# Performance work log

Measured on AMD Instinct MI355X. Metric: run time of the kernel, lower is better.

## Reference

```python
import jax, jax.numpy as jnp
import numpy as np
import math

B, S, E, A, H, L, V = 2, 2048, 512, 512, 8, 4, 50257
HD = A // H  # 64 per-head dim (attention_size // n_heads)
PAD = 0
EPS = 1e-5

def _sin_pe():
    pos = np.arange(S)[:, None].astype(np.float32)
    div = np.exp(np.arange(0, E, 2).astype(np.float32) * (-math.log(10000.0) / E))
    pe = np.zeros((S, E), dtype=np.float32)
    pe[:, 0::2] = np.sin(pos * div)
    pe[:, 1::2] = np.cos(pos * div)
    return jnp.asarray(pe)

PE = _sin_pe()

def setup_inputs():
    key = jax.random.key(0)
    ks = jax.random.split(key, 20)
    s = 0.02
    emb = jax.random.normal(ks[0], (V, E), jnp.float32) * s
    emb = emb.at[PAD].set(0.0)  # nn.Embedding padding_idx row is zero
    return {
        "input_ids": jax.random.randint(ks[1], (B, S), 0, V, dtype=jnp.int32),
        "attention_mask": jnp.ones((B, S), jnp.int32),
        "emb": emb,
        "Wq": jax.random.normal(ks[2], (L, H, E, HD), jnp.float32) * s,
        "Wk": jax.random.normal(ks[3], (L, H, E, HD), jnp.float32) * s,
        "Wv": jax.random.normal(ks[4], (L, H, E, HD), jnp.float32) * s,
        "Wo": jax.random.normal(ks[5], (L, A, E), jnp.float32) * s,
        "ln1_g": jnp.ones((L, E), jnp.float32),
        "ln1_b": jnp.zeros((L, E), jnp.float32),
        "ln2_g": jnp.ones((L, E), jnp.float32),
        "ln2_b": jnp.zeros((L, E), jnp.float32),
        "ff_w1": jax.random.normal(ks[6], (L, E, 4 * E), jnp.float32) * s,
        "ff_b1": jnp.zeros((L, 4 * E), jnp.float32),
        "ff_w2": jax.random.normal(ks[7], (L, 4 * E, E), jnp.float32) * s,
        "ff_b2": jnp.zeros((L, E), jnp.float32),
        "lnf_g": jnp.ones((E,), jnp.float32),
        "lnf_b": jnp.zeros((E,), jnp.float32),
        "Wout": jax.random.normal(ks[8], (E, V), jnp.float32) * s,
        "bout": jnp.zeros((V,), jnp.float32),
    }

def _ln(x, g, b):
    m = jnp.mean(x, axis=-1, keepdims=True)
    v = jnp.mean((x - m) ** 2, axis=-1, keepdims=True)
    return (x - m) / jnp.sqrt(v + EPS) * g + b

def reference(input_ids, attention_mask, emb, Wq, Wk, Wv, Wo, ln1_g, ln1_b, ln2_g, ln2_b, ff_w1, ff_b1, ff_w2, ff_b2, lnf_g, lnf_b, Wout, bout):
    # mask: padding (attention_mask==0) broadcast over queries, OR causal upper triangle
    pad = (attention_mask == 0)[:, None, :]                  # [B,1,S]
    causal = jnp.triu(jnp.ones((S, S), bool), 1)             # [S,S]
    mask = (pad | causal)[:, None, :, :]                     # [B,1,S,S]
    x = emb[input_ids] + PE[None, :S]                        # [B,S,E]
    scale = 1.0 / math.sqrt(HD)

    def block(x, p):
        wq, wk, wv, wo, g1, b1, g2, b2, w1, c1, w2, c2 = p
        xn = _ln(x, g1, b1)
        q = jnp.einsum('bse,hed->bhsd', xn, wq)
        k = jnp.einsum('bse,hed->bhsd', xn, wk)
        v = jnp.einsum('bse,hed->bhsd', xn, wv)
        scores = jnp.einsum('bhsd,bhtd->bhst', q, k) * scale  # masked_fill(-inf) then /sqrt(dk) == mask after scale
        scores = jnp.where(mask, -jnp.inf, scores)
        p_attn = jax.nn.softmax(scores, axis=-1)
        attn = jnp.einsum('bhst,bhtd->bhsd', p_attn, v)
        attn = attn.transpose(0, 2, 1, 3).reshape(B, S, A)    # concat heads
        x = x + attn @ wo                                     # residual + out proj (no bias)
        xn2 = _ln(x, g2, b2)
        h = jax.nn.gelu(xn2 @ w1 + c1, approximate=False)     # nn.GELU default (erf)
        x = x + h @ w2 + c2
        return x, None

    params = (Wq, Wk, Wv, Wo, ln1_g, ln1_b, ln2_g, ln2_b, ff_w1, ff_b1, ff_w2, ff_b2)
    x, _ = jax.lax.scan(block, x, params)
    return _ln(x, lnf_g, lnf_b) @ Wout + bout                 # [B,S,V]
```

## Files before the change

### kernel.cpp

```cpp
#include <hip/hip_runtime.h>
#include <math.h>

#define BB 2
#define SS 2048
#define EE 512
#define HH 8
#define HD 64
#define LL 4
#define VV 50257
#define NTOK (BB*SS)
#define VPAD2 50432

typedef __bf16 bf16_t;
typedef bf16_t bf16x8 __attribute__((ext_vector_type(8)));
typedef float  f32x4  __attribute__((ext_vector_type(4)));

__device__ __forceinline__ void gload_lds16(const void* g, void* l) {
  __builtin_amdgcn_global_load_lds(
      (const __attribute__((address_space(1))) void*)g,
      (__attribute__((address_space(3))) void*)l, 16, 0, 0);
}

__global__ __launch_bounds__(256) void embed_ln_kernel(
    const int* __restrict__ ids, const float* __restrict__ emb,
    const float* __restrict__ g, const float* __restrict__ b,
    float* __restrict__ x, bf16_t* __restrict__ xn) {
  int wv = threadIdx.x >> 6, lane = threadIdx.x & 63;
  int row = blockIdx.x * 4 + wv;
  int s = row & (SS - 1);
  int id = ids[row];
  const float* er = emb + (size_t)id * EE;
  float v[8];
  float sum = 0.f;
#pragma unroll
  for (int j = 0; j < 8; j++) {
    int e = lane * 8 + j;
    float freq = __expf((float)(e & ~1) * -0.01798894604f);
    float ang  = (float)s * freq;
    float pe   = (e & 1) ? __cosf(ang) : __sinf(ang);
    v[j] = er[e] + pe;
    sum += v[j];
  }
  float4* xp = reinterpret_cast<float4*>(x + (size_t)row * EE + lane * 8);
  xp[0] = make_float4(v[0], v[1], v[2], v[3]);
  xp[1] = make_float4(v[4], v[5], v[6], v[7]);
#pragma unroll
  for (int o = 32; o > 0; o >>= 1) sum += __shfl_xor(sum, o);
  float mean = sum * (1.f / EE);
  float var = 0.f;
#pragma unroll
  for (int j = 0; j < 8; j++) { float d = v[j] - mean; var += d * d; }
#pragma unroll
  for (int o = 32; o > 0; o >>= 1) var += __shfl_xor(var, o);
  float inv = rsqrtf(var * (1.f / EE) + 1e-5f);
  bf16_t tmp[8];
#pragma unroll
  for (int j = 0; j < 8; j++) {
    int e = lane * 8 + j;
    tmp[j] = (bf16_t)((v[j] - mean) * inv * g[e] + b[e]);
  }
  *reinterpret_cast<bf16x8*>(xn + (size_t)row * EE + lane * 8) = *reinterpret_cast<bf16x8*>(tmp);
}

__global__ __launch_bounds__(256) void ln_kernel(const float* __restrict__ in,
                                                 bf16_t* __restrict__ out,
                                                 const float* __restrict__ g,
                                                 const float* __restrict__ b) {
  int wv = threadIdx.x >> 6, lane = threadIdx.x & 63;
  int row = blockIdx.x * 4 + wv;
  const float4* r = reinterpret_cast<const float4*>(in + (size_t)row * EE) + lane * 2;
  float4 v0 = r[0], v1 = r[1];
  float s = v0.x + v0.y + v0.z + v0.w + v1.x + v1.y + v1.z + v1.w;
#pragma unroll
  for (int o = 32; o > 0; o >>= 1) s += __shfl_xor(s, o);
  float mean = s * (1.f / EE);
  float d0 = v0.x-mean, d1 = v0.y-mean, d2 = v0.z-mean, d3 = v0.w-mean;
  float d4 = v1.x-mean, d5 = v1.y-mean, d6 = v1.z-mean, d7 = v1.w-mean;
  float var = d0*d0+d1*d1+d2*d2+d3*d3+d4*d4+d5*d5+d6*d6+d7*d7;
#pragma unroll
  for (int o = 32; o > 0; o >>= 1) var += __shfl_xor(var, o);
  float inv = rsqrtf(var * (1.f / EE) + 1e-5f);
  const float4* gp = reinterpret_cast<const float4*>(g) + lane * 2;
  const float4* bp = reinterpret_cast<const float4*>(b) + lane * 2;
  float4 g0 = gp[0], g1 = gp[1], b0 = bp[0], b1 = bp[1];
  bf16_t tmp[8];
  tmp[0] = (bf16_t)(d0*inv*g0.x + b0.x); tmp[1] = (bf16_t)(d1*inv*g0.y + b0.y);
  tmp[2] = (bf16_t)(d2*inv*g0.z + b0.z); tmp[3] = (bf16_t)(d3*inv*g0.w + b0.w);
  tmp[4] = (bf16_t)(d4*inv*g1.x + b1.x); tmp[5] = (bf16_t)(d5*inv*g1.y + b1.y);
  tmp[6] = (bf16_t)(d6*inv*g1.z + b1.z); tmp[7] = (bf16_t)(d7*inv*g1.w + b1.w);
  *reinterpret_cast<bf16x8*>(out + (size_t)row * EE + lane * 8) = *reinterpret_cast<bf16x8*>(tmp);
}

__device__ __forceinline__ void transpose_tile(const float* __restrict__ ip,
                                               bf16_t* __restrict__ op,
                                               int k0, int n0, int ldin, int ldout,
                                               int Nvalid, float* T) {
  int t = threadIdx.x;
  int r = t >> 2, cb = (t & 3) * 16;
#pragma unroll
  for (int i = 0; i < 16; i++) {
    int n = n0 + cb + i;
    T[r * 65 + cb + i] = (n < Nvalid) ? ip[(size_t)(k0 + r) * ldin + n] : 0.f;
  }
  __syncthreads();
  bf16_t tmp[16];
#pragma unroll
  for (int i = 0; i < 16; i++) tmp[i] = (bf16_t)T[(cb + i) * 65 + r];
  bf16_t* o = op + (size_t)(n0 + r) * ldout + k0 + cb;
  *reinterpret_cast<bf16x8*>(o)     = *reinterpret_cast<bf16x8*>(&tmp[0]);
  *reinterpret_cast<bf16x8*>(o + 8) = *reinterpret_cast<bf16x8*>(&tmp[8]);
}

__global__ __launch_bounds__(256) void wconv_all(
    const float* __restrict__ Wq, const float* __restrict__ Wk,
    const float* __restrict__ Wv, const float* __restrict__ Wo,
    const float* __restrict__ fw1, const float* __restrict__ fw2,
    const float* __restrict__ Wout,
    bf16_t* Wqkv, bf16_t* WoT, bf16_t* W1T, bf16_t* W2T, bf16_t* WoutT) {
  __shared__ float T[64 * 65];
  int bid = blockIdx.x;
  if (bid < 768) {
    int kx = bid & 7, z = bid >> 3;
    int l = z / 24, rem = z % 24, sec = rem >> 3, h = rem & 7;
    const float* W = sec == 0 ? Wq : (sec == 1 ? Wk : Wv);
    const float* ip = W + (size_t)(l * 8 + h) * (EE * HD);
    bf16_t* op = Wqkv + (size_t)l * (1536 * 512) + (size_t)(sec * 512 + h * 64) * 512;
    transpose_tile(ip, op, kx * 64, 0, HD, EE, HD, T);
  } else if (bid < 1024) {
    int r = bid - 768;
    int kx = r & 7, ny = (r >> 3) & 7, l = r >> 6;
    transpose_tile(Wo + (size_t)l * 512 * 512, WoT + (size_t)l * 512 * 512,
                   kx * 64, ny * 64, 512, 512, 512, T);
  } else if (bid < 2048) {
    int r = bid - 1024;
    int kx = r & 7, ny = (r >> 3) & 31, l = r >> 8;
    transpose_tile(fw1 + (size_t)l * 512 * 2048, W1T + (size_t)l * 2048 * 512,
                   kx * 64, ny * 64, 2048, 512, 2048, T);
  } else if (bid < 3072) {
    int r = bid - 2048;
    int kx = r & 31, ny = (r >> 5) & 7, l = r >> 8;
    transpose_tile(fw2 + (size_t)l * 2048 * 512, W2T + (size_t)l * 512 * 2048,
                   kx * 64, ny * 64, 512, 2048, 512, T);
  } else {
    int r = bid - 3072;
    int kx = r & 7, ny = r >> 3;
    transpose_tile(Wout, WoutT, kx * 64, ny * 64, VV, 512, VV, T);
  }
}

template<int MODE, int TM>
__global__ __launch_bounds__(256) void gemm_bf16(
    const bf16_t* __restrict__ A, const bf16_t* __restrict__ Bt,
    int M, int N, int K,
    const float* __restrict__ bias,
    float* __restrict__ Cf, bf16_t* __restrict__ Cb,
    bf16_t* __restrict__ qo, bf16_t* __restrict__ ko, bf16_t* __restrict__ vo) {
  constexpr int MI = TM / 32;
  constexpr int LW = MI + 4;
  __shared__ __align__(16) bf16_t As[2][TM * 64];
  __shared__ __align__(16) bf16_t Bs[2][128 * 64];
  int tid = threadIdx.x, lane = tid & 63, w = tid >> 6;
  int lr = lane & 15, lg = lane >> 4;
  int m0 = blockIdx.y * TM, n0 = blockIdx.x * 128;
  f32x4 acc[MI][4];
#pragma unroll
  for (int i = 0; i < MI; i++)
#pragma unroll
    for (int j = 0; j < 4; j++) acc[i][j] = (f32x4){0.f, 0.f, 0.f, 0.f};
  int wr = w >> 1, wc = w & 1;

  const bf16_t* Abase = A  + (size_t)(m0 + lr) * K + lg * 8;
  const bf16_t* Bbase = Bt + (size_t)(n0 + lr) * K + lg * 8;

  auto stage = [&](int buf, int k0) {
#pragma unroll
    for (int i = 0; i < MI; i++) {
      int c = w * MI + i;
      gload_lds16(Abase + (size_t)(c >> 1) * 16 * K + k0 + (c & 1) * 32,
                  (char*)&As[buf][0] + c * 1024);
    }
#pragma unroll
    for (int i = 0; i < 4; i++) {
      int c = w * 4 + i;
      gload_lds16(Bbase + (size_t)(c >> 1) * 16 * K + k0 + (c & 1) * 32,
                  (char*)&Bs[buf][0] + c * 1024);
    }
  };

  int nk = K >> 6;
  stage(0, 0);
  for (int k = 0; k < nk; k++) {
    int cur = k & 1;
    if (k + 1 < nk) {
      stage(cur ^ 1, (k + 1) << 6);
      asm volatile("s_waitcnt vmcnt(%0)" :: "i"(LW) : "memory");
    } else {
      asm volatile("s_waitcnt vmcnt(0)" ::: "memory");
    }
    __builtin_amdgcn_s_barrier();
    __builtin_amdgcn_s_setprio(1);
#pragma unroll
    for (int kk = 0; kk < 2; kk++) {
      bf16x8 afr[MI], bfr[4];
#pragma unroll
      for (int mi = 0; mi < MI; mi++)
        afr[mi] = *reinterpret_cast<const bf16x8*>(
            &As[cur][(((wr * MI + mi) << 1) + kk) * 512 + lane * 8]);
#pragma unroll
      for (int ni = 0; ni < 4; ni++)
        bfr[ni] = *reinterpret_cast<const bf16x8*>(
            &Bs[cur][(((wc * 4 + ni) << 1) + kk) * 512 + lane * 8]);
#pragma unroll
      for (int mi = 0; mi < MI; mi++)
#pragma unroll
        for (int ni = 0; ni < 4; ni++)
          acc[mi][ni] = __builtin_amdgcn_mfma_f32_16x16x32_bf16(afr[mi], bfr[ni], acc[mi][ni], 0, 0, 0);
    }
    __builtin_amdgcn_s_setprio(0);
    __builtin_amdgcn_s_barrier();
  }

#pragma unroll
  for (int mi = 0; mi < MI; mi++)
#pragma unroll
    for (int ni = 0; ni < 4; ni++) {
      int colg = n0 + wc * 64 + ni * 16 + lr;
#pragma unroll
      for (int j = 0; j < 4; j++) {
        int rowg = m0 + wr * (TM / 2) + mi * 16 + lg * 4 + j;
        float v = acc[mi][ni][j];
        if (MODE == 0) {
          int sec = colg >> 9, cc = colg & 511, hh = cc >> 6, dd = cc & 63;
          int bi = rowg >> 11, s = rowg & 2047;
          if (sec == 0)      qo[(((size_t)bi * HH + hh) * SS + s) * HD + dd] = (bf16_t)(v * 0.125f);
          else if (sec == 1) ko[(((size_t)bi * HH + hh) * SS + s) * HD + dd] = (bf16_t)v;
          else               vo[(((size_t)bi * HH + hh) * HD + dd) * SS + s] = (bf16_t)v;
        } else if (MODE == 1) {
          v += bias[colg];
          v = 0.5f * v * (1.f + erff(v * 0.70710678f));
          Cb[(size_t)rowg * N + colg] = (bf16_t)v;
        } else {
          if (bias) v += bias[colg];
          Cf[(size_t)rowg * EE + colg] += v;
        }
      }
    }
}

__global__ __launch_bounds__(512) void gemm256_out(
    const bf16_t* __restrict__ A, const bf16_t* __restrict__ Bt,
    const float* __restrict__ bias, float* __restrict__ C) {
  __shared__ __align__(16) char smem[64 * 260 * 4];
  bf16_t* As = (bf16_t*)smem;
  bf16_t* Bs = (bf16_t*)(smem + 32768);
  float*  Ep = (float*)smem;
  int tid = threadIdx.x, lane = tid & 63, w = tid >> 6;
  int lr = lane & 15, lg = lane >> 4;
  int bid = blockIdx.x;
  int n0 = (bid % 197) * 256, m0 = (bid / 197) * 256;
  int wr = w >> 2, wc = w & 3;
  f32x4 acc[8][4];
#pragma unroll
  for (int i = 0; i < 8; i++)
#pragma unroll
    for (int j = 0; j < 4; j++) acc[i][j] = (f32x4){0.f, 0.f, 0.f, 0.f};

  const bf16_t* Abase = A  + (size_t)(m0 + lr) * 512 + lg * 8;
  const bf16_t* Bbase = Bt + (size_t)(n0 + lr) * 512 + lg * 8;

  for (int k0 = 0; k0 < 512; k0 += 64) {
#pragma unroll
    for (int i = 0; i < 4; i++) {
      int c = w * 4 + i;
      gload_lds16(Abase + (size_t)(c >> 1) * 16 * 512 + k0 + (c & 1) * 32,
                  (char*)As + c * 1024);
      gload_lds16(Bbase + (size_t)(c >> 1) * 16 * 512 + k0 + (c & 1) * 32,
                  (char*)Bs + c * 1024);
    }
    __syncthreads();
#pragma unroll
    for (int kk = 0; kk < 2; kk++) {
      bf16x8 afr[8], bfr[4];
#pragma unroll
      for (int mi = 0; mi < 8; mi++)
        afr[mi] = *reinterpret_cast<const bf16x8*>(
            &As[(((wr * 8 + mi) << 1) + kk) * 512 + lane * 8]);
#pragma unroll
      for (int ni = 0; ni < 4; ni++)
        bfr[ni] = *reinterpret_cast<const bf16x8*>(
            &Bs[(((wc * 4 + ni) << 1) + kk) * 512 + lane * 8]);
#pragma unroll
      for (int mi = 0; mi < 8; mi++)
#pragma unroll
        for (int ni = 0; ni < 4; ni++)
          acc[mi][ni] = __builtin_amdgcn_mfma_f32_16x16x32_bf16(afr[mi], bfr[ni], acc[mi][ni], 0, 0, 0);
    }
    __syncthreads();
  }

  int colBase = n0 + (tid & 63) * 4;
  float b0 = 0.f, b1 = 0.f, b2 = 0.f, b3 = 0.f;
  if (colBase + 3 < VV) {
    float4 bv = *reinterpret_cast<const float4*>(bias + colBase);
    b0 = bv.x; b1 = bv.y; b2 = bv.z; b3 = bv.w;
  } else {
    if (colBase     < VV) b0 = bias[colBase];
    if (colBase + 1 < VV) b1 = bias[colBase + 1];
    if (colBase + 2 < VV) b2 = bias[colBase + 2];
  }
  int rw = tid >> 6;
  for (int ch = 0; ch < 4; ch++) {
    __syncthreads();
    if (wr == (ch >> 1)) {
      int mib = (ch & 1) * 4;
#pragma unroll
      for (int mi2 = 0; mi2 < 4; mi2++)
#pragma unroll
        for (int ni = 0; ni < 4; ni++) {
          int col = wc * 64 + ni * 16 + lr;
#pragma unroll
          for (int j = 0; j < 4; j++)
            Ep[(mi2 * 16 + lg * 4 + j) * 260 + col] = acc[mib + mi2][ni][j];
        }
    }
    __syncthreads();
#pragma unroll
    for (int pass = 0; pass < 8; pass++) {
      int r = pass * 8 + rw;
      f32x4 v = *reinterpret_cast<const f32x4*>(&Ep[r * 260 + (tid & 63) * 4]);
      v[0] += b0; v[1] += b1; v[2] += b2; v[3] += b3;
      float* dst = &C[(size_t)(m0 + ch * 64 + r) * VV + colBase];
      if (colBase + 3 < VV) {
        __builtin_nontemporal_store(v, reinterpret_cast<f32x4*>(dst));
      } else {
        if (colBase     < VV) __builtin_nontemporal_store(v[0], dst);
        if (colBase + 1 < VV) __builtin_nontemporal_store(v[1], dst + 1);
        if (colBase + 2 < VV) __builtin_nontemporal_store(v[2], dst + 2);
      }
    }
  }
}

#define QBLK 64
#define KVB 64
__global__ __launch_bounds__(256) void attn_kernel(
    const bf16_t* __restrict__ qb, const bf16_t* __restrict__ kb,
    const bf16_t* __restrict__ vT, const int* __restrict__ amask,
    bf16_t* __restrict__ ab) {
  __shared__ bf16_t Qs[QBLK][72];
  __shared__ bf16_t Ps[QBLK][72];
  __shared__ __align__(16) bf16_t Ks[2][KVB * 64];
  __shared__ __align__(16) bf16_t Vs[2][KVB * 64];
  int tid = threadIdx.x, lane = tid & 63, w = tid >> 6;
  int lr = lane & 15, lg = lane >> 4;
  int bid = blockIdx.x;
  int bh = bid & 15;
  int qi = bid >> 4;
  int qq = (qi < 16) ? qi : 47 - qi;
  int q0 = qq * QBLK;
  int b = bh >> 3, h = bh & 7;
  const bf16_t* Qg = qb + (size_t)bh * SS * HD;
  const bf16_t* Kg = kb + (size_t)bh * SS * HD;
  const bf16_t* Vg = vT + (size_t)bh * HD * SS;
  const int* am = amask + b * SS;

  {
    int r = tid >> 2, c = (tid & 3) * 16;
    const uint4* s = reinterpret_cast<const uint4*>(Qg + (size_t)(q0 + r) * HD + c);
    uint4 a0 = s[0], a1 = s[1];
    *reinterpret_cast<uint4*>(&Qs[r][c])     = a0;
    *reinterpret_cast<uint4*>(&Qs[r][c + 8]) = a1;
  }

  auto stageKV = [&](int buf, int kv0) {
#pragma unroll
    for (int i = 0; i < 4; i++) {
      int c = w * 4 + i;
      if (c < 8) {
        gload_lds16(Kg + (size_t)(kv0 + (c >> 1) * 16 + lr) * HD + (c & 1) * 32 + lg * 8,
                    (char*)&Ks[buf][0] + c * 1024);
      } else {
        int cc = c - 8;
        gload_lds16(Vg + (size_t)((cc >> 1) * 16 + lr) * SS + kv0 + (cc & 1) * 32 + lg * 8,
                    (char*)&Vs[buf][0] + cc * 1024);
      }
    }
  };

  f32x4 o[4];
  f32x4 m_run, l_run;
  m_run = (f32x4){-1e30f, -1e30f, -1e30f, -1e30f};
  l_run = (f32x4){0.f, 0.f, 0.f, 0.f};
#pragma unroll
  for (int nd = 0; nd < 4; nd++) o[nd] = (f32x4){0.f, 0.f, 0.f, 0.f};

  stageKV(0, 0);
  __syncthreads();

  int ntile = qq + 1;
  for (int t = 0; t < ntile; t++) {
    int buf = t & 1;
    int kv0 = t * KVB;
    if (t + 1 < ntile) stageKV(buf ^ 1, kv0 + KVB);

    f32x4 sc[4];
#pragma unroll
    for (int ni = 0; ni < 4; ni++) sc[ni] = (f32x4){0.f, 0.f, 0.f, 0.f};
#pragma unroll
    for (int kk = 0; kk < 2; kk++) {
      bf16x8 af = *reinterpret_cast<const bf16x8*>(&Qs[w * 16 + lr][kk * 32 + lg * 8]);
      bf16x8 bf[4];
#pragma unroll
      for (int ni = 0; ni < 4; ni++)
        bf[ni] = *reinterpret_cast<const bf16x8*>(&Ks[buf][((ni << 1) + kk) * 512 + lane * 8]);
#pragma unroll
      for (int ni = 0; ni < 4; ni++)
        sc[ni] = __builtin_amdgcn_mfma_f32_16x16x32_bf16(af, bf[ni], sc[ni], 0, 0, 0);
    }

    {
      int qrb = q0 + w * 16 + lg * 4;
      float kmv[4];
#pragma unroll
      for (int ni = 0; ni < 4; ni++) kmv[ni] = am[kv0 + ni * 16 + lr] ? 0.f : -1e30f;
#pragma unroll
      for (int ni = 0; ni < 4; ni++) {
        int kg = kv0 + ni * 16 + lr;
#pragma unroll
        for (int j = 0; j < 4; j++) {
          float s = sc[ni][j] + kmv[ni];
          sc[ni][j] = (kg <= qrb + j) ? s : -1e30f;
        }
      }
      f32x4 rmax = sc[0];
#pragma unroll
      for (int ni = 1; ni < 4; ni++)
#pragma unroll
        for (int j = 0; j < 4; j++) rmax[j] = fmaxf(rmax[j], sc[ni][j]);
#pragma unroll
      for (int msk = 1; msk <= 8; msk <<= 1)
#pragma unroll
        for (int j = 0; j < 4; j++) rmax[j] = fmaxf(rmax[j], __shfl_xor(rmax[j], msk));
      f32x4 mnew, corr;
#pragma unroll
      for (int j = 0; j < 4; j++) {
        mnew[j] = fmaxf(m_run[j], rmax[j]);
        corr[j] = __expf(m_run[j] - mnew[j]);
      }
      m_run = mnew;
      f32x4 rs = (f32x4){0.f, 0.f, 0.f, 0.f};
#pragma unroll
      for (int ni = 0; ni < 4; ni++) {
#pragma unroll
        for (int j = 0; j < 4; j++) {
          float p = __expf(sc[ni][j] - mnew[j]);
          rs[j] += p;
          Ps[w * 16 + lg * 4 + j][ni * 16 + lr] = (bf16_t)p;
        }
      }
#pragma unroll
      for (int msk = 1; msk <= 8; msk <<= 1)
#pragma unroll
        for (int j = 0; j < 4; j++) rs[j] += __shfl_xor(rs[j], msk);
#pragma unroll
      for (int j = 0; j < 4; j++) l_run[j] = l_run[j] * corr[j] + rs[j];
#pragma unroll
      for (int nd = 0; nd < 4; nd++) o[nd] = o[nd] * corr;
    }

#pragma unroll
    for (int kc = 0; kc < 2; kc++) {
      bf16x8 pa = *reinterpret_cast<const bf16x8*>(&Ps[w * 16 + lr][kc * 32 + lg * 8]);
      bf16x8 vb[4];
#pragma unroll
      for (int nd = 0; nd < 4; nd++)
        vb[nd] = *reinterpret_cast<const bf16x8*>(&Vs[buf][((nd << 1) + kc) * 512 + lane * 8]);
#pragma unroll
      for (int nd = 0; nd < 4; nd++)
        o[nd] = __builtin_amdgcn_mfma_f32_16x16x32_bf16(pa, vb[nd], o[nd], 0, 0, 0);
    }
    asm volatile("s_waitcnt vmcnt(0)" ::: "memory");
    asm volatile("s_barrier" ::: "memory");
  }

  f32x4 linv;
#pragma unroll
  for (int j = 0; j < 4; j++) linv[j] = 1.f / l_run[j];
#pragma unroll
  for (int nd = 0; nd < 4; nd++)
#pragma unroll
    for (int j = 0; j < 4; j++) {
      int rowg = b * SS + q0 + w * 16 + lg * 4 + j;
      int col = h * HD + nd * 16 + lr;
      ab[(size_t)rowg * EE + col] = (bf16_t)(o[nd][j] * linv[j]);
    }
}

extern "C" void kernel_launch(void* const* d_in, const int* in_sizes, int n_in,
                              void* d_out, int out_size, void* d_ws, size_t ws_size,
                              hipStream_t stream) {
  const int*   ids   = (const int*)d_in[0];
  const int*   amask = (const int*)d_in[1];
  const float* emb   = (const float*)d_in[2];
  const float* Wq    = (const float*)d_in[3];
  const float* Wk    = (const float*)d_in[4];
  const float* Wv    = (const float*)d_in[5];
  const float* Wo    = (const float*)d_in[6];
  const float* ln1g  = (const float*)d_in[7];
  const float* ln1b  = (const float*)d_in[8];
  const float* ln2g  = (const float*)d_in[9];
  const float* ln2b  = (const float*)d_in[10];
  const float* fw1   = (const float*)d_in[11];
  const float* fb1   = (const float*)d_in[12];
  const float* fw2   = (const float*)d_in[13];
  const float* fb2   = (const float*)d_in[14];
  const float* lnfg  = (const float*)d_in[15];
  const float* lnfb  = (const float*)d_in[16];
  const float* Wout  = (const float*)d_in[17];
  const float* bout  = (const float*)d_in[18];
  float* out = (float*)d_out;

  float*  x     = (float*)d_ws;
  bf16_t* xn    = (bf16_t*)((char*)d_ws + (8u << 20));
  bf16_t* WoutT = (bf16_t*)((char*)d_ws + (12u << 20));
  char* sc = (char*)d_out;
  bf16_t* qbuf = (bf16_t*)(sc);
  bf16_t* kbuf = (bf16_t*)(sc + 4194304);
  bf16_t* vTb  = (bf16_t*)(sc + 8388608);
  bf16_t* ab   = (bf16_t*)(sc + 12582912);
  bf16_t* hb   = (bf16_t*)(sc + 16777216);
  bf16_t* Wqkv = (bf16_t*)(sc + 33554432);
  bf16_t* WoT  = (bf16_t*)(sc + 39845888);
  bf16_t* W1T  = (bf16_t*)(sc + 41943040);
  bf16_t* W2T  = (bf16_t*)(sc + 50331648);

  wconv_all<<<dim3(3072 + 8 * (VPAD2 / 64)), 256, 0, stream>>>(
      Wq, Wk, Wv, Wo, fw1, fw2, Wout, Wqkv, WoT, W1T, W2T, WoutT);

  embed_ln_kernel<<<NTOK / 4, 256, 0, stream>>>(ids, emb, ln1g, ln1b, x, xn);

  for (int l = 0; l < LL; l++) {
    if (l > 0)
      ln_kernel<<<NTOK / 4, 256, 0, stream>>>(x, xn, ln1g + l * EE, ln1b + l * EE);
    gemm_bf16<0, 64><<<dim3(12, 64), 256, 0, stream>>>(xn, Wqkv + (size_t)l * 1536 * 512,
        NTOK, 1536, 512, nullptr, nullptr, nullptr, qbuf, kbuf, vTb);
    attn_kernel<<<dim3(512), 256, 0, stream>>>(qbuf, kbuf, vTb, amask, ab);
    gemm_bf16<2, 32><<<dim3(4, 128), 256, 0, stream>>>(ab, WoT + (size_t)l * 512 * 512,
        NTOK, 512, 512, nullptr, x, nullptr, nullptr, nullptr, nullptr);
    ln_kernel<<<NTOK / 4, 256, 0, stream>>>(x, xn, ln2g + l * EE, ln2b + l * EE);
    gemm_bf16<1, 64><<<dim3(16, 64), 256, 0, stream>>>(xn, W1T + (size_t)l * 2048 * 512,
        NTOK, 2048, 512, fb1 + l * 2048, nullptr, hb, nullptr, nullptr, nullptr);
    gemm_bf16<2, 32><<<dim3(4, 128), 256, 0, stream>>>(hb, W2T + (size_t)l * 512 * 2048,
        NTOK, 512, 2048, fb2 + l * EE, x, nullptr, nullptr, nullptr, nullptr);
  }
  ln_kernel<<<NTOK / 4, 256, 0, stream>>>(x, xn, lnfg, lnfb);
  gemm256_out<<<dim3(16 * (VPAD2 / 256)), 512, 0, stream>>>(xn, WoutT, bout, out);
}
```

Baseline: 1.290 ms.

## Triple-buffer LDS staging in QKV/FFN1 GEMMs and attention KV loads

Adds a gemm3_64 kernel with three LDS buffers and a prefetch distance of two, used for the QKV projection and the FFN up-projection. The attention kernel's K/V staging moves from double to triple buffering, waiting with a partial vmcnt instead of draining all loads each tile. The key padding mask is precomputed into shared memory once per block instead of being read from global memory every tile. The aim is better overlap of global-to-LDS loads with MFMA work, at the cost of more LDS per block and possibly lower occupancy.

Result: no change. 1.279 ms, median of 3 (-0.8%).

```diff
diff --git a/kernel.cpp b/kernel.cpp
--- a/kernel.cpp
+++ b/kernel.cpp
@@ -148,13 +148,103 @@
   }
 }
 
+template<int MODE>
+__global__ __launch_bounds__(256) void gemm3_64(
+    const bf16_t* __restrict__ A, const bf16_t* __restrict__ Bt,
+    int M, int N, int K,
+    const float* __restrict__ bias, bf16_t* __restrict__ Cb,
+    bf16_t* __restrict__ qo, bf16_t* __restrict__ ko, bf16_t* __restrict__ vo) {
+  constexpr int TM = 64, MI = 2;
+  __shared__ __align__(16) bf16_t As[3][TM * 64];
+  __shared__ __align__(16) bf16_t Bs[3][128 * 64];
+  int tid = threadIdx.x, lane = tid & 63, w = tid >> 6;
+  int lr = lane & 15, lg = lane >> 4;
+  int m0 = blockIdx.y * TM, n0 = blockIdx.x * 128;
+  f32x4 acc[MI][4];
+#pragma unroll
+  for (int i = 0; i < MI; i++)
+#pragma unroll
+    for (int j = 0; j < 4; j++) acc[i][j] = (f32x4){0.f, 0.f, 0.f, 0.f};
+  int wr = w >> 1, wc = w & 1;
+
+  const bf16_t* Abase = A  + (size_t)(m0 + lr) * K + lg * 8;
+  const bf16_t* Bbase = Bt + (size_t)(n0 + lr) * K + lg * 8;
+
+  auto stage = [&](int buf, int k0) {
+#pragma unroll
+    for (int i = 0; i < MI; i++) {
+      int c = w * MI + i;
+      gload_lds16(Abase + (size_t)(c >> 1) * 16 * K + k0 + (c & 1) * 32,
+                  (char*)&As[buf][0] + c * 1024);
+    }
+#pragma unroll
+    for (int i = 0; i < 4; i++) {
+      int c = w * 4 + i;
+      gload_lds16(Bbase + (size_t)(c >> 1) * 16 * K + k0 + (c & 1) * 32,
+                  (char*)&Bs[buf][0] + c * 1024);
+    }
+  };
+
+  int nk = K >> 6;
+  stage(0, 0);
+  if (nk > 1) stage(1, 64);
+  for (int k = 0; k < nk; k++) {
+    int cur = k % 3;
+    if (k + 1 < nk) asm volatile("s_waitcnt vmcnt(6)" ::: "memory");
+    else            asm volatile("s_waitcnt vmcnt(0)" ::: "memory");
+    __builtin_amdgcn_s_barrier();
+    __builtin_amdgcn_s_setprio(1);
+#pragma unroll
+    for (int kk = 0; kk < 2; kk++) {
+      bf16x8 afr[MI], bfr[4];
+#pragma unroll
+      for (int mi = 0; mi < MI; mi++)
+        afr[mi] = *reinterpret_cast<const bf16x8*>(
+            &As[cur][(((wr * MI + mi) << 1) + kk) * 512 + lane * 8]);
+#pragma unroll
+      for (int ni = 0; ni < 4; ni++)
+        bfr[ni] = *reinterpret_cast<const bf16x8*>(
+            &Bs[cur][(((wc * 4 + ni) << 1) + kk) * 512 + lane * 8]);
+#pragma unroll
+      for (int mi = 0; mi < MI; mi++)
+#pragma unroll
+        for (int ni = 0; ni < 4; ni++)
+          acc[mi][ni] = __builtin_amdgcn_mfma_f32_16x16x32_bf16(afr[mi], bfr[ni], acc[mi][ni], 0, 0, 0);
+    }
+    __builtin_amdgcn_s_setprio(0);
+    if (k + 2 < nk) stage((k + 2) % 3, (k + 2) << 6);
+  }
+
+#pragma unroll
+  for (int mi = 0; mi < MI; mi++)
+#pragma unroll
+    for (int ni = 0; ni < 4; ni++) {
+      int colg = n0 + wc * 64 + ni * 16 + lr;
+#pragma unroll
+      for (int j = 0; j < 4; j++) {
+        int rowg = m0 + wr * (TM / 2) + mi * 16 + lg * 4 + j;
+        float v = acc[mi][ni][j];
+        if (MODE == 0) {
+          int sec = colg >> 9, cc = colg & 511, hh = cc >> 6, dd = cc & 63;
+          int bi = rowg >> 11, s = rowg & 2047;
+          if (sec == 0)      qo[(((size_t)bi * HH + hh) * SS + s) * HD + dd] = (bf16_t)(v * 0.125f);
+          else if (sec == 1) ko[(((size_t)bi * HH + hh) * SS + s) * HD + dd] = (bf16_t)v;
+          else               vo[(((size_t)bi * HH + hh) * HD + dd) * SS + s] = (bf16_t)v;
+        } else {
+          v += bias[colg];
+          v = 0.5f * v * (1.f + erff(v * 0.70710678f));
+          Cb[(size_t)rowg * N + colg] = (bf16_t)v;
+        }
+      }
+    }
+}
+
 template<int MODE, int TM>
 __global__ __launch_bounds__(256) void gemm_bf16(
     const bf16_t* __restrict__ A, const bf16_t* __restrict__ Bt,
     int M, int N, int K,
     const float* __restrict__ bias,
-    float* __restrict__ Cf, bf16_t* __restrict__ Cb,
-    bf16_t* __restrict__ qo, bf16_t* __restrict__ ko, bf16_t* __restrict__ vo) {
+    float* __restrict__ Cf, bf16_t* __restrict__ Cb) {
   constexpr int MI = TM / 32;
   constexpr int LW = MI + 4;
   __shared__ __align__(16) bf16_t As[2][TM * 64];
@@ -229,20 +319,8 @@
       for (int j = 0; j < 4; j++) {
         int rowg = m0 + wr * (TM / 2) + mi * 16 + lg * 4 + j;
         float v = acc[mi][ni][j];
-        if (MODE == 0) {
-          int sec = colg >> 9, cc = colg & 511, hh = cc >> 6, dd = cc & 63;
-          int bi = rowg >> 11, s = rowg & 2047;
-          if (sec == 0)      qo[(((size_t)bi * HH + hh) * SS + s) * HD + dd] = (bf16_t)(v * 0.125f);
-          else if (sec == 1) ko[(((size_t)bi * HH + hh) * SS + s) * HD + dd] = (bf16_t)v;
-          else               vo[(((size_t)bi * HH + hh) * HD + dd) * SS + s] = (bf16_t)v;
-        } else if (MODE == 1) {
-          v += bias[colg];
-          v = 0.5f * v * (1.f + erff(v * 0.70710678f));
-          Cb[(size_t)rowg * N + colg] = (bf16_t)v;
-        } else {
-          if (bias) v += bias[colg];
-          Cf[(size_t)rowg * EE + colg] += v;
-        }
+        if (bias) v += bias[colg];
+        Cf[(size_t)rowg * EE + colg] += v;
       }
     }
 }
@@ -349,8 +427,9 @@
     bf16_t* __restrict__ ab) {
   __shared__ bf16_t Qs[QBLK][72];
   __shared__ bf16_t Ps[QBLK][72];
-  __shared__ __align__(16) bf16_t Ks[2][KVB * 64];
-  __shared__ __align__(16) bf16_t Vs[2][KVB * 64];
+  __shared__ __align__(16) bf16_t Ks[3][KVB * 64];
+  __shared__ __align__(16) bf16_t Vs[3][KVB * 64];
+  __shared__ float kmAll[SS];
   int tid = threadIdx.x, lane = tid & 63, w = tid >> 6;
   int lr = lane & 15, lg = lane >> 4;
   int bid = blockIdx.x;
@@ -362,7 +441,6 @@
   const bf16_t* Qg = qb + (size_t)bh * SS * HD;
   const bf16_t* Kg = kb + (size_t)bh * SS * HD;
   const bf16_t* Vg = vT + (size_t)bh * HD * SS;
-  const int* am = amask + b * SS;
 
   {
     int r = tid >> 2, c = (tid & 3) * 16;
@@ -370,6 +448,11 @@
     uint4 a0 = s[0], a1 = s[1];
     *reinterpret_cast<uint4*>(&Qs[r][c])     = a0;
     *reinterpret_cast<uint4*>(&Qs[r][c + 8]) = a1;
+  }
+#pragma unroll
+  for (int i = 0; i < 8; i++) {
+    int s = i * 256 + tid;
+    kmAll[s] = amask[b * SS + s] ? 0.f : -1e30f;
   }
 
   auto stageKV = [&](int buf, int kv0) {
@@ -394,14 +477,17 @@
 #pragma unroll
   for (int nd = 0; nd < 4; nd++) o[nd] = (f32x4){0.f, 0.f, 0.f, 0.f};
 
+  int ntile = qq + 1;
   stageKV(0, 0);
+  if (ntile > 1) stageKV(1, KVB);
   __syncthreads();
 
-  int ntile = qq + 1;
   for (int t = 0; t < ntile; t++) {
-    int buf = t & 1;
+    int buf = t % 3;
     int kv0 = t * KVB;
-    if (t + 1 < ntile) stageKV(buf ^ 1, kv0 + KVB);
+    if (t + 1 < ntile) asm volatile("s_waitcnt vmcnt(4)" ::: "memory");
+    else               asm volatile("s_waitcnt vmcnt(0)" ::: "memory");
+    __builtin_amdgcn_s_barrier();
 
     f32x4 sc[4];
 #pragma unroll
@@ -422,7 +508,7 @@
       int qrb = q0 + w * 16 + lg * 4;
       float kmv[4];
 #pragma unroll
-      for (int ni = 0; ni < 4; ni++) kmv[ni] = am[kv0 + ni * 16 + lr] ? 0.f : -1e30f;
+      for (int ni = 0; ni < 4; ni++) kmv[ni] = kmAll[kv0 + ni * 16 + lr];
 #pragma unroll
       for (int ni = 0; ni < 4; ni++) {
         int kg = kv0 + ni * 16 + lr;
@@ -479,8 +565,8 @@
       for (int nd = 0; nd < 4; nd++)
         o[nd] = __builtin_amdgcn_mfma_f32_16x16x32_bf16(pa, vb[nd], o[nd], 0, 0, 0);
     }
-    asm volatile("s_waitcnt vmcnt(0)" ::: "memory");
-    asm volatile("s_barrier" ::: "memory");
+
+    if (t + 2 < ntile) stageKV((t + 2) % 3, kv0 + 2 * KVB);
   }
 
   f32x4 linv;
@@ -542,16 +628,16 @@
   for (int l = 0; l < LL; l++) {
     if (l > 0)
       ln_kernel<<<NTOK / 4, 256, 0, stream>>>(x, xn, ln1g + l * EE, ln1b + l * EE);
-    gemm_bf16<0, 64><<<dim3(12, 64), 256, 0, stream>>>(xn, Wqkv + (size_t)l * 1536 * 512,
-        NTOK, 1536, 512, nullptr, nullptr, nullptr, qbuf, kbuf, vTb);
+    gemm3_64<0><<<dim3(12, 64), 256, 0, stream>>>(xn, Wqkv + (size_t)l * 1536 * 512,
+        NTOK, 1536, 512, nullptr, nullptr, qbuf, kbuf, vTb);
     attn_kernel<<<dim3(512), 256, 0, stream>>>(qbuf, kbuf, vTb, amask, ab);
     gemm_bf16<2, 32><<<dim3(4, 128), 256, 0, stream>>>(ab, WoT + (size_t)l * 512 * 512,
-        NTOK, 512, 512, nullptr, x, nullptr, nullptr, nullptr, nullptr);
+        NTOK, 512, 512, nullptr, x, nullptr);
     ln_kernel<<<NTOK / 4, 256, 0, stream>>>(x, xn, ln2g + l * EE, ln2b + l * EE);
-    gemm_bf16<1, 64><<<dim3(16, 64), 256, 0, stream>>>(xn, W1T + (size_t)l * 2048 * 512,
-        NTOK, 2048, 512, fb1 + l * 2048, nullptr, hb, nullptr, nullptr, nullptr);
+    gemm3_64<1><<<dim3(16, 64), 256, 0, stream>>>(xn, W1T + (size_t)l * 2048 * 512,
+        NTOK, 2048, 512, fb1 + l * 2048, hb, nullptr, nullptr, nullptr);
     gemm_bf16<2, 32><<<dim3(4, 128), 256, 0, stream>>>(hb, W2T + (size_t)l * 512 * 2048,
-        NTOK, 512, 2048, fb2 + l * EE, x, nullptr, nullptr, nullptr, nullptr);
+        NTOK, 512, 2048, fb2 + l * EE, x, nullptr);
   }
   ln_kernel<<<NTOK / 4, 256, 0, stream>>>(x, xn, lnfg, lnfb);
   gemm256_out<<<dim3(16 * (VPAD2 / 256)), 512, 0, stream>>>(xn, WoutT, bout, out);
```
